# Optimization experiments

Hardware: AMD Instinct MI355X
Metric: run time of the kernel (lower is better)

## Reference

```python
import jax, jax.numpy as jnp
import numpy as np

N_NODES = 50000


def _degree_norms(edge_index, n_nodes):
    # PyG GCNConv: add self-loops, deg = 1 + in-degree at target (col)
    src, dst = edge_index[0], edge_index[1]
    deg = 1.0 + jax.ops.segment_sum(jnp.ones(src.shape[0], jnp.float32), dst,
                                    num_segments=n_nodes)
    d_inv_sqrt = 1.0 / jnp.sqrt(deg)  # deg >= 1 always (self-loop)
    norm_e = d_inv_sqrt[src] * d_inv_sqrt[dst]   # per-edge sym norm
    norm_self = d_inv_sqrt * d_inv_sqrt          # self-loop weight
    return norm_e, norm_self


def _gcn_conv(x, W, b, src, dst, norm_e, norm_self, n_nodes):
    h = x @ W                                    # [N, F_out]
    msg = h[src] * norm_e[:, None]               # gather + scale, [E, F_out]
    agg = jax.ops.segment_sum(msg, dst, num_segments=n_nodes)
    return agg + norm_self[:, None] * h + b


def setup_inputs() -> dict:
    key = jax.random.key(0)
    ks = jax.random.split(key, 10)
    F_in, H = 128, 128
    E = 1_600_000
    x = jax.random.normal(ks[0], (N_NODES, F_in), jnp.float32)
    edge_index = jax.random.randint(ks[1], (2, E), 0, N_NODES, dtype=jnp.int64)

    def glorot(k, fi, fo):
        s = jnp.sqrt(6.0 / (fi + fo)).astype(jnp.float32)
        return jax.random.uniform(k, (fi, fo), jnp.float32, -s, s)

    return {
        "x": x,
        "edge_index": edge_index,
        "W1": glorot(ks[2], F_in, H), "b1": jnp.zeros((H,), jnp.float32),
        "W2": glorot(ks[3], H, H),    "b2": jnp.zeros((H,), jnp.float32),
        "W3": glorot(ks[4], H, H),    "b3": jnp.zeros((H,), jnp.float32),
        "W4": glorot(ks[5], H, 1),    "b4": jnp.zeros((1,), jnp.float32),
    }


def reference(x, edge_index, W1, b1, W2, b2, W3, b3, W4, b4):
    src, dst = edge_index[0], edge_index[1]
    norm_e, norm_self = _degree_norms(edge_index, N_NODES)
    h = jax.nn.relu(_gcn_conv(x, W1, b1, src, dst, norm_e, norm_self, N_NODES))
    h = jax.nn.relu(_gcn_conv(h, W2, b2, src, dst, norm_e, norm_self, N_NODES))
    h = jax.nn.relu(_gcn_conv(h, W3, b3, src, dst, norm_e, norm_self, N_NODES))
    return _gcn_conv(h, W4, b4, src, dst, norm_e, norm_self, N_NODES)
```

## Files before the change

### kernel.cpp

```cpp
#include <hip/hip_runtime.h>
#include <hip/hip_bf16.h>
#include <stdint.h>

typedef unsigned int u32;
typedef unsigned short u16;

#define F 128

typedef __attribute__((ext_vector_type(8))) short bf16x8;
typedef __attribute__((ext_vector_type(8))) u16 u16x8;
typedef __attribute__((ext_vector_type(4))) float f32x4;

__device__ __forceinline__ float bf2f(u16 v){
  union { u32 u; float f; } x; x.u = ((u32)v) << 16; return x.f;
}
__device__ __forceinline__ float bflo(u32 w){
  union { u32 u; float f; } x; x.u = w << 16; return x.f;
}
__device__ __forceinline__ float bfhi(u32 w){
  union { u32 u; float f; } x; x.u = w & 0xFFFF0000u; return x.f;
}
__device__ __forceinline__ u16 f2bf(float f){
  union { float f; u32 u; } x; x.f = f;
  u32 u = x.u;
  return (u16)((u + 0x7fffu + ((u >> 16) & 1u)) >> 16);
}

__global__ void k_flags(const u32* __restrict__ xw, const u32* __restrict__ ei,
                        int* __restrict__ flags){
  if (blockIdx.x == 0){
    u32 hit = 0;
    for (int i = threadIdx.x; i < 2048; i += 256){
      u32 e = (xw[i] >> 7) & 0xFFu;
      if (e > 160u) hit = 1;
    }
    if (hit) atomicOr(&flags[1], 1);
  } else {
    u32 v = 0;
    for (int i = threadIdx.x; i < 4096; i += 256) v |= ei[2*i + 1];
    if (v) atomicOr(&flags[0], 1);
  }
}

__launch_bounds__(256)
__global__ void k_bhist(const u32* __restrict__ w, int E, const int* __restrict__ flagp,
                        int NB, int* __restrict__ bcnt){
  __shared__ int h[256];
  int st = (*flagp) ? 1 : 2;
  int t = threadIdx.x;
  h[t] = 0;
  __syncthreads();
  int base = blockIdx.x*4096;
  #pragma unroll 4
  for (int k = 0; k < 16; k++){
    int i = base + k*256 + t;
    if (i < E){
      int d = (int)w[(size_t)(E + i)*st];
      atomicAdd(&h[d >> 8], 1);
    }
  }
  __syncthreads();
  if (t < NB && h[t]) atomicAdd(&bcnt[t], h[t]);
}

__global__ void k_bscan(const int* __restrict__ bcnt, int NB, int E,
                        int* __restrict__ bbase, int* __restrict__ bump){
  __shared__ int s[256];
  int t = threadIdx.x;
  int v = (t < NB) ? bcnt[t] : 0;
  s[t] = v;
  __syncthreads();
  for (int off = 1; off < 256; off <<= 1){
    int x = (t >= off) ? s[t - off] : 0;
    __syncthreads();
    s[t] += x;
    __syncthreads();
  }
  bbase[t] = s[t] - v;
  if (t == 255) bbase[256] = E;
  bump[t] = 0;
}

__launch_bounds__(256)
__global__ void k_msplit(const u32* __restrict__ w, int E, const int* __restrict__ flagp,
                         const int* __restrict__ bbase, int* __restrict__ bump,
                         u32* __restrict__ ebuf){
  __shared__ int h[256];
  __shared__ int cb[256];
  int st = (*flagp) ? 1 : 2;
  int t = threadIdx.x;
  h[t] = 0;
  __syncthreads();
  int base = blockIdx.x*4096;
  u32 ps[16]; int bk[16]; int rk[16];
  #pragma unroll 4
  for (int k = 0; k < 16; k++){
    int i = base + k*256 + t;
    if (i < E){
      u32 s = w[(size_t)i*st];
      u32 d = w[(size_t)(E + i)*st];
      bk[k] = (int)(d >> 8);
      ps[k] = (s & 0xFFFFu) | ((d & 0xFFu) << 16);
      rk[k] = atomicAdd(&h[bk[k]], 1);
    } else bk[k] = -1;
  }
  __syncthreads();
  cb[t] = h[t] ? (bbase[t] + atomicAdd(&bump[t], h[t])) : 0;
  __syncthreads();
  #pragma unroll 4
  for (int k = 0; k < 16; k++){
    if (bk[k] >= 0) ebuf[cb[bk[k]] + rk[k]] = ps[k];
  }
}

__launch_bounds__(256)
__global__ void k_bemit(const u32* __restrict__ ebuf, const int* __restrict__ bbase,
                        int N, int* __restrict__ deg, int* __restrict__ rs,
                        u32* __restrict__ csr32, float* __restrict__ dis){
  __shared__ int nd[256];
  __shared__ int nofs[256];
  __shared__ int s[256];
  int b = blockIdx.x;
  int t = threadIdx.x;
  int e0 = bbase[b], e1 = bbase[b + 1];
  int pb = e0 + b*1024;
  nd[t] = 0;
  __syncthreads();
  for (int i = e0 + t; i < e1; i += 256) atomicAdd(&nd[ebuf[i] >> 16], 1);
  __syncthreads();
  int v = nd[t];
  int pv = (v + 3) & ~3;
  s[t] = pv;
  __syncthreads();
  for (int off = 1; off < 256; off <<= 1){
    int x = (t >= off) ? s[t - off] : 0;
    __syncthreads();
    s[t] += x;
    __syncthreads();
  }
  nofs[t] = s[t] - pv;
  int node = b*256 + t;
  if (node < N){
    deg[node] = v;
    rs[node]  = pb + nofs[t];
    dis[node] = rsqrtf(1.0f + (float)v);
  }
  nd[t] = 0;
  __syncthreads();
  for (int i = e0 + t; i < e1; i += 256){
    u32 p = ebuf[i];
    int d = (int)(p >> 16);
    int pos = pb + nofs[d] + atomicAdd(&nd[d], 1);
    csr32[pos] = (p & 0xFFFFu) << 6;
  }
}

__global__ void k_prep(const void* b1, const void* b2, const void* b3,
                       const void* W4, const void* b4, const int* __restrict__ isf32,
                       float* __restrict__ bb, float* __restrict__ wf4,
                       float* __restrict__ bb4){
  int t = threadIdx.x;
  int f32 = *isf32;
  if (t < 384){
    const void* s = (t < 128) ? b1 : ((t < 256) ? b2 : b3);
    int i = t & 127;
    bb[t] = f32 ? ((const float*)s)[i] : bf2f(((const u16*)s)[i]);
  } else if (t < 512){
    int i = t - 384;
    wf4[i] = f32 ? ((const float*)W4)[i] : bf2f(((const u16*)W4)[i]);
  } else if (t == 512){
    bb4[0] = f32 ? ((const float*)b4)[0] : bf2f(((const u16*)b4)[0]);
  }
}

__global__ void k_cvt_b(const void* __restrict__ in, const int* __restrict__ isf32,
                        u16* __restrict__ out, int N){
  int i = blockIdx.x*256 + threadIdx.x;
  if (i >= N*16) return;
  int r = i >> 4, part = i & 15;
  u16x8 o;
  if (*isf32){
    const f32x4* p = (const f32x4*)in + (size_t)i*2;
    f32x4 v0 = p[0], v1 = p[1];
    #pragma unroll
    for (int k = 0; k < 4; k++){ o[k] = f2bf(v0[k]); o[k+4] = f2bf(v1[k]); }
  } else {
    o = *((const u16x8*)in + i);
  }
  int slice = part >> 2, elem = (part & 3)*8;
  __builtin_nontemporal_store(o, (u16x8*)(out + ((size_t)slice*N + r)*32 + elem));
}

__global__ void k_swz3(const void* W1, const void* W2, const void* W3,
                       const int* __restrict__ isf32, u16* __restrict__ WL){
  int l = blockIdx.x >> 6;
  const void* W = (l == 0) ? W1 : ((l == 1) ? W2 : W3);
  int idx = (blockIdx.x & 63)*256 + threadIdx.x;
  int j    = idx & 7;
  int lane = (idx >> 3) & 63;
  int kb   = (idx >> 9) & 3;
  int ct   = idx >> 11;
  int m = lane & 15, q = lane >> 4;
  int k = kb*32 + q*8 + j;
  int c = ct*16 + m;
  float v = (*isf32) ? ((const float*)W)[k*F + c] : bf2f(((const u16*)W)[k*F + c]);
  WL[l*16384 + idx] = f2bf(v);
}

__launch_bounds__(256)
__global__ void k_mm(const u16* __restrict__ X, const u16* __restrict__ WL,
                     const float* __restrict__ dis, u16* __restrict__ G, int N){
  int w = threadIdx.x >> 6, lane = threadIdx.x & 63;
  int m = lane & 15, q = lane >> 4;
  int row0 = blockIdx.x*64 + w*16;
  int arow = row0 + m;
  bf16x8 a[4];
  if (arow < N){
    #pragma unroll
    for (int kb = 0; kb < 4; kb++)
      a[kb] = *(const bf16x8*)(X + ((size_t)kb*N + arow)*32 + q*8);
  } else {
    #pragma unroll
    for (int kb = 0; kb < 4; kb++) a[kb] = (bf16x8){0,0,0,0,0,0,0,0};
  }
  f32x4 acc[8];
  #pragma unroll
  for (int ct = 0; ct < 8; ct++) acc[ct] = (f32x4){0.f,0.f,0.f,0.f};
  #pragma unroll
  for (int ct = 0; ct < 8; ct++){
    #pragma unroll
    for (int kb = 0; kb < 4; kb++){
      bf16x8 b = *(const bf16x8*)(WL + ((size_t)((ct*4 + kb)*64 + lane))*8);
      acc[ct] = __builtin_amdgcn_mfma_f32_16x16x32_bf16(a[kb], b, acc[ct], 0, 0, 0);
    }
  }
  int rbase = row0 + q*4;
  #pragma unroll
  for (int r = 0; r < 4; r++){
    int row = rbase + r;
    if (row < N){
      float dv = dis[row];
      #pragma unroll
      for (int ct = 0; ct < 8; ct++)
        __builtin_nontemporal_store(f2bf(dv*acc[ct][r]),
            &G[((size_t)(ct >> 1)*(N+1) + row)*32 + (ct & 1)*16 + m]);
    }
  }
}

__launch_bounds__(256)
__global__ void k_agg(const u16* __restrict__ G, const float* __restrict__ dis,
                      const int* __restrict__ rs, const int* __restrict__ deg,
                      const u32* __restrict__ csr32, const float* __restrict__ bias,
                      u16* __restrict__ Xout, int N, int relu){
  int b = blockIdx.x;
  int c = (b & 7) >> 1;
  int wv = threadIdx.x >> 6;
  int lane = threadIdx.x & 63;
  int slot = lane >> 4, fp = lane & 15;
  int wid0 = (b >> 3)*16 + (b & 1)*8 + wv;
  const char* Gs = (const char*)G + (size_t)c*(size_t)(N+1)*64;
  const char* Cb = (const char*)csr32;
  u32 zoff = ((u32)N) << 6;
  u32 fo   = ((u32)fp) << 2;
  float bv0 = bias[c*32 + 2*fp], bv1 = bias[c*32 + 2*fp + 1];

  #pragma unroll 2
  for (int t = 0; t < 2; t++){
    int wid = wid0 + 4*t;
    if (wid >= N) break;
    int base = rs[wid], len = deg[wid];
    float a0 = 0.f, a1 = 0.f;
    if (len > 0){
      u32 coff = ((u32)base << 2) + ((u32)slot << 4);
      int nfull = len >> 4, rem = len & 15;
      uint4 q = *(const uint4*)(Cb + coff); coff += 64;
      for (int s = 0; s < nfull; s++){
        uint4 qn = *(const uint4*)(Cb + coff); coff += 64;
        u32 w0 = *(const u32*)(Gs + (q.x + fo));
        u32 w1 = *(const u32*)(Gs + (q.y + fo));
        u32 w2 = *(const u32*)(Gs + (q.z + fo));
        u32 w3 = *(const u32*)(Gs + (q.w + fo));
        a0 += bflo(w0); a1 += bfhi(w0);
        a0 += bflo(w1); a1 += bfhi(w1);
        a0 += bflo(w2); a1 += bfhi(w2);
        a0 += bflo(w3); a1 += bfhi(w3);
        q = qn;
      }
      if (rem){
        int sb = slot << 2;
        u32 o0 = ((sb + 0 < rem) ? q.x : zoff) + fo;
        u32 o1 = ((sb + 1 < rem) ? q.y : zoff) + fo;
        u32 o2 = ((sb + 2 < rem) ? q.z : zoff) + fo;
        u32 o3 = ((sb + 3 < rem) ? q.w : zoff) + fo;
        u32 w0 = *(const u32*)(Gs + o0);
        u32 w1 = *(const u32*)(Gs + o1);
        u32 w2 = *(const u32*)(Gs + o2);
        u32 w3 = *(const u32*)(Gs + o3);
        a0 += bflo(w0); a1 += bfhi(w0);
        a0 += bflo(w1); a1 += bfhi(w1);
        a0 += bflo(w2); a1 += bfhi(w2);
        a0 += bflo(w3); a1 += bfhi(w3);
      }
    }
    a0 += __shfl_xor(a0, 16, 64); a0 += __shfl_xor(a0, 32, 64);
    a1 += __shfl_xor(a1, 16, 64); a1 += __shfl_xor(a1, 32, 64);
    if (slot == 0){
      u32 sw = *(const u32*)(Gs + ((((u32)wid) << 6) + fo));
      a0 += bflo(sw); a1 += bfhi(sw);
      float dv = dis[wid];
      float o0 = fmaf(dv, a0, bv0);
      float o1 = fmaf(dv, a1, bv1);
      if (relu){ o0 = fmaxf(o0, 0.f); o1 = fmaxf(o1, 0.f); }
      u32 pk = (u32)f2bf(o0) | ((u32)f2bf(o1) << 16);
      __builtin_nontemporal_store(pk,
          (u32*)((char*)Xout + (size_t)c*N*64 + (((size_t)wid) << 6) + fo));
    }
  }
}

__global__ void k_mm4(const u16* __restrict__ X, const float* __restrict__ W4f,
                      const float* __restrict__ dis, float* __restrict__ G4, int N){
  int gt   = blockIdx.x*blockDim.x + threadIdx.x;
  int wid  = gt >> 6;
  int lane = threadIdx.x & 63;
  if (wid >= N) return;
  u32 xw = *(const u32*)(X + ((size_t)(lane >> 4)*N + wid)*32 + 2*(lane & 15));
  float acc = bflo(xw)*W4f[2*lane] + bfhi(xw)*W4f[2*lane + 1];
  #pragma unroll
  for (int off = 32; off > 0; off >>= 1) acc += __shfl_down(acc, off, 64);
  if (lane == 0) G4[wid] = dis[wid]*acc;
}

__global__ void k_agg4(const float* __restrict__ G4, const float* __restrict__ dis,
                       const int* __restrict__ rs, const int* __restrict__ deg,
                       const u32* __restrict__ csr32, const float* __restrict__ b4f,
                       const int* __restrict__ isf32, void* __restrict__ out, int N){
  int i = blockIdx.x*blockDim.x + threadIdx.x;
  if (i >= N) return;
  int base = rs[i], len = deg[i];
  const char* Gb = (const char*)G4;
  float a0 = 0.f, a1 = 0.f, a2 = 0.f, a3 = 0.f;
  int j = 0;
  for (; j + 4 <= len; j += 4){
    u32 e0 = csr32[base + j],     e1 = csr32[base + j + 1];
    u32 e2 = csr32[base + j + 2], e3 = csr32[base + j + 3];
    a0 += *(const float*)(Gb + (e0 >> 4));
    a1 += *(const float*)(Gb + (e1 >> 4));
    a2 += *(const float*)(Gb + (e2 >> 4));
    a3 += *(const float*)(Gb + (e3 >> 4));
  }
  for (; j < len; j++) a0 += *(const float*)(Gb + (csr32[base + j] >> 4));
  float r = dis[i]*(G4[i] + ((a0 + a1) + (a2 + a3))) + b4f[0];
  if (*isf32) ((float*)out)[i] = r;
  else        ((u16*)out)[i]   = f2bf(r);
}

extern "C" void kernel_launch(void* const* d_in, const int* in_sizes, int n_in,
                              void* d_out, int out_size, void* d_ws, size_t ws_size,
                              hipStream_t stream){
  const void* x0 = d_in[0];
  const u32*  ei = (const u32*)d_in[1];
  const void* Wp[4] = {d_in[2], d_in[4], d_in[6], d_in[8]};
  const void* bp[4] = {d_in[3], d_in[5], d_in[7], d_in[9]};
  int N = in_sizes[0] / F;
  int E = in_sizes[1] / 2;
  int NB = (N + 255) >> 8;

  char* base = (char*)d_ws;
  size_t off = 0;
  auto alloc = [&](size_t bytes)->char*{
    char* p = base + off;
    off = (off + bytes + 255) & ~(size_t)255;
    return p;
  };
  int*   deg  = (int*)  alloc((size_t)N*4);
  float* dis  = (float*)alloc((size_t)N*4);
  int*   rs   = (int*)  alloc((size_t)N*4);
  float* g4   = (float*)alloc((size_t)N*4);
  int*   bcnt = (int*)  alloc(1024);
  int*   bbase= (int*)  alloc(1056);
  int*   bump = (int*)  alloc(1024);
  int*   flags= (int*)  alloc(256);
  u32*   ebuf = (u32*)  alloc((size_t)E*4);
  u32*   csr32= (u32*)  alloc(((size_t)E + (size_t)NB*1024 + 64)*4);
  u16*   WL   = (u16*)  alloc(3*16384*2);
  float* wf4  = (float*)alloc(F*4);
  float* bb   = (float*)alloc(3*F*4);
  float* bb4  = (float*)alloc(256);
  u16*   gbuf = (u16*)  alloc((size_t)4*(N+1)*64);
  u16*   xbuf = (u16*)  alloc((size_t)N*F*2);

  hipMemsetAsync(bcnt, 0, 1024, stream);
  hipMemsetAsync(flags, 0, 256, stream);
  for (int c = 0; c < 4; c++)
    hipMemsetAsync(gbuf + ((size_t)c*(N+1) + N)*32, 0, 64, stream);

  int* eflag = flags + 0;
  int* isf32 = flags + 1;

  int nbt = (N + 255)/256;
  int etb = (E + 4095)/4096;

  k_flags <<<2, 256, 0, stream>>>((const u32*)x0, ei, flags);
  k_bhist <<<etb, 256, 0, stream>>>(ei, E, eflag, NB, bcnt);
  k_bscan <<<1, 256, 0, stream>>>(bcnt, NB, E, bbase, bump);
  k_msplit<<<etb, 256, 0, stream>>>(ei, E, eflag, bbase, bump, ebuf);
  k_bemit <<<NB, 256, 0, stream>>>(ebuf, bbase, N, deg, rs, csr32, dis);
  k_prep  <<<1, 640, 0, stream>>>(bp[0], bp[1], bp[2], Wp[3], bp[3], isf32, bb, wf4, bb4);
  k_swz3  <<<192, 256, 0, stream>>>(Wp[0], Wp[1], Wp[2], isf32, WL);
  k_cvt_b <<<(N*16 + 255)/256, 256, 0, stream>>>(x0, isf32, xbuf, N);

  int mmb  = (N + 63)/64;
  int aggB = ((N + 15)/16)*8;

  for (int l = 0; l < 3; l++){
    k_mm <<<mmb, 256, 0, stream>>>(xbuf, WL + l*16384, dis, gbuf, N);
    k_agg<<<aggB, 256, 0, stream>>>(gbuf, dis, rs, deg, csr32, bb + l*F, xbuf, N, 1);
  }
  k_mm4 <<<((size_t)N*64 + 255)/256, 256, 0, stream>>>(xbuf, wf4, dis, g4, N);
  k_agg4<<<nbt, 256, 0, stream>>>(g4, dis, rs, deg, csr32, bb4, isf32, (void*)d_out, N);
}
```

Before: 412.8 us.

## Pad CSR rows to 32, widen aggregation gathers with dot2, fuse input conversion

CSR rows are padded to multiples of 32 with zero-row sentinels and interleaved, so the aggregation kernel can skip remainder handling. Each lane now gathers 8 bytes (four bf16 features) and accumulates with v_dot2_f32_bf16, which halves the lanes per feature slice and adds an extra shuffle reduction stage. The separate input conversion kernel is removed and the first matmul reads raw fp32 or bf16 x directly. The cost is extra padded gathers on low-degree nodes, since average degree is about 32, and a larger CSR buffer.

```diff
diff --git a/kernel.cpp b/kernel.cpp
--- a/kernel.cpp
+++ b/kernel.cpp
@@ -10,20 +10,22 @@
 typedef __attribute__((ext_vector_type(8))) short bf16x8;
 typedef __attribute__((ext_vector_type(8))) u16 u16x8;
 typedef __attribute__((ext_vector_type(4))) float f32x4;
+typedef __attribute__((ext_vector_type(2))) u32 u32x2;
+typedef __attribute__((ext_vector_type(4))) u32 u32x4;
 
 __device__ __forceinline__ float bf2f(u16 v){
   union { u32 u; float f; } x; x.u = ((u32)v) << 16; return x.f;
-}
-__device__ __forceinline__ float bflo(u32 w){
-  union { u32 u; float f; } x; x.u = w << 16; return x.f;
-}
-__device__ __forceinline__ float bfhi(u32 w){
-  union { u32 u; float f; } x; x.u = w & 0xFFFF0000u; return x.f;
 }
 __device__ __forceinline__ u16 f2bf(float f){
   union { float f; u32 u; } x; x.f = f;
   u32 u = x.u;
   return (u16)((u + 0x7fffu + ((u >> 16) & 1u)) >> 16);
+}
+__device__ __forceinline__ bf16x8 as_bf(u16x8 v){
+  union { u16x8 a; bf16x8 b; } u; u.a = v; return u.b;
+}
+__device__ __forceinline__ void d2(float& a, u32 w, u32 sel){
+  asm("v_dot2_f32_bf16 %0, %1, %2, %0" : "+v"(a) : "v"(w), "v"(sel));
 }
 
 __global__ void k_flags(const u32* __restrict__ xw, const u32* __restrict__ ei,
@@ -123,13 +125,13 @@
   int b = blockIdx.x;
   int t = threadIdx.x;
   int e0 = bbase[b], e1 = bbase[b + 1];
-  int pb = e0 + b*1024;
+  int pb = ((e0 + 31) & ~31) + b*8192;
   nd[t] = 0;
   __syncthreads();
   for (int i = e0 + t; i < e1; i += 256) atomicAdd(&nd[ebuf[i] >> 16], 1);
   __syncthreads();
   int v = nd[t];
-  int pv = (v + 3) & ~3;
+  int pv = (v + 31) & ~31;
   s[t] = pv;
   __syncthreads();
   for (int off = 1; off < 256; off <<= 1){
@@ -150,8 +152,15 @@
   for (int i = e0 + t; i < e1; i += 256){
     u32 p = ebuf[i];
     int d = (int)(p >> 16);
-    int pos = pb + nofs[d] + atomicAdd(&nd[d], 1);
+    int rr = atomicAdd(&nd[d], 1);
+    int pos = pb + nofs[d] + (rr & ~31) + ((rr & 7) << 2) + ((rr >> 3) & 3);
     csr32[pos] = (p & 0xFFFFu) << 6;
+  }
+  u32 zv = ((u32)N) << 6;
+  int bme = pb + nofs[t];
+  for (int rr = v; rr < pv; rr++){
+    int pos = bme + (rr & ~31) + ((rr & 7) << 2) + ((rr >> 3) & 3);
+    csr32[pos] = zv;
   }
 }
 
@@ -173,24 +182,6 @@
   }
 }
 
-__global__ void k_cvt_b(const void* __restrict__ in, const int* __restrict__ isf32,
-                        u16* __restrict__ out, int N){
-  int i = blockIdx.x*256 + threadIdx.x;
-  if (i >= N*16) return;
-  int r = i >> 4, part = i & 15;
-  u16x8 o;
-  if (*isf32){
-    const f32x4* p = (const f32x4*)in + (size_t)i*2;
-    f32x4 v0 = p[0], v1 = p[1];
-    #pragma unroll
-    for (int k = 0; k < 4; k++){ o[k] = f2bf(v0[k]); o[k+4] = f2bf(v1[k]); }
-  } else {
-    o = *((const u16x8*)in + i);
-  }
-  int slice = part >> 2, elem = (part & 3)*8;
-  __builtin_nontemporal_store(o, (u16x8*)(out + ((size_t)slice*N + r)*32 + elem));
-}
-
 __global__ void k_swz3(const void* W1, const void* W2, const void* W3,
                        const int* __restrict__ isf32, u16* __restrict__ WL){
   int l = blockIdx.x >> 6;
@@ -208,20 +199,40 @@
 }
 
 __launch_bounds__(256)
-__global__ void k_mm(const u16* __restrict__ X, const u16* __restrict__ WL,
-                     const float* __restrict__ dis, u16* __restrict__ G, int N){
+__global__ void k_mm(const u16* __restrict__ X, const void* __restrict__ Xraw,
+                     const int* __restrict__ isf32, const u16* __restrict__ WL,
+                     const float* __restrict__ dis, u16* __restrict__ G,
+                     int N, int mode){
   int w = threadIdx.x >> 6, lane = threadIdx.x & 63;
   int m = lane & 15, q = lane >> 4;
   int row0 = blockIdx.x*64 + w*16;
   int arow = row0 + m;
-  bf16x8 a[4];
+  u16x8 a[4];
   if (arow < N){
-    #pragma unroll
-    for (int kb = 0; kb < 4; kb++)
-      a[kb] = *(const bf16x8*)(X + ((size_t)kb*N + arow)*32 + q*8);
+    if (mode == 0){
+      #pragma unroll
+      for (int kb = 0; kb < 4; kb++)
+        a[kb] = *(const u16x8*)(X + ((size_t)kb*N + arow)*32 + q*8);
+    } else if (*isf32){
+      const float* xp = (const float*)Xraw + (size_t)arow*F;
+      #pragma unroll
+      for (int kb = 0; kb < 4; kb++){
+        f32x4 v0 = *(const f32x4*)(xp + kb*32 + q*8);
+        f32x4 v1 = *(const f32x4*)(xp + kb*32 + q*8 + 4);
+        u16x8 o;
+        #pragma unroll
+        for (int k = 0; k < 4; k++){ o[k] = f2bf(v0[k]); o[k+4] = f2bf(v1[k]); }
+        a[kb] = o;
+      }
+    } else {
+      const u16* xp = (const u16*)Xraw + (size_t)arow*F;
+      #pragma unroll
+      for (int kb = 0; kb < 4; kb++)
+        a[kb] = *(const u16x8*)(xp + kb*32 + q*8);
+    }
   } else {
     #pragma unroll
-    for (int kb = 0; kb < 4; kb++) a[kb] = (bf16x8){0,0,0,0,0,0,0,0};
+    for (int kb = 0; kb < 4; kb++) a[kb] = (u16x8){0,0,0,0,0,0,0,0};
   }
   f32x4 acc[8];
   #pragma unroll
@@ -230,8 +241,8 @@
   for (int ct = 0; ct < 8; ct++){
     #pragma unroll
     for (int kb = 0; kb < 4; kb++){
-      bf16x8 b = *(const bf16x8*)(WL + ((size_t)((ct*4 + kb)*64 + lane))*8);
-      acc[ct] = __builtin_amdgcn_mfma_f32_16x16x32_bf16(a[kb], b, acc[ct], 0, 0, 0);
+      bf16x8 bfr = *(const bf16x8*)(WL + ((size_t)((ct*4 + kb)*64 + lane))*8);
+      acc[ct] = __builtin_amdgcn_mfma_f32_16x16x32_bf16(as_bf(a[kb]), bfr, acc[ct], 0, 0, 0);
     }
   }
   int rbase = row0 + q*4;
@@ -255,66 +266,73 @@
                       u16* __restrict__ Xout, int N, int relu){
   int b = blockIdx.x;
   int c = (b & 7) >> 1;
-  int wv = threadIdx.x >> 6;
   int lane = threadIdx.x & 63;
-  int slot = lane >> 4, fp = lane & 15;
-  int wid0 = (b >> 3)*16 + (b & 1)*8 + wv;
+  int slot = lane >> 3, fp = lane & 7;
+  int wid0 = (b >> 3)*16 + (b & 1)*8 + (threadIdx.x >> 6);
   const char* Gs = (const char*)G + (size_t)c*(size_t)(N+1)*64;
   const char* Cb = (const char*)csr32;
-  u32 zoff = ((u32)N) << 6;
-  u32 fo   = ((u32)fp) << 2;
-  float bv0 = bias[c*32 + 2*fp], bv1 = bias[c*32 + 2*fp + 1];
+  u32 fo = ((u32)fp) << 3;
+  u32 sel_lo = 0x00003F80u;
+  u32 sel_hi = 0x3F800000u;
 
   #pragma unroll 2
   for (int t = 0; t < 2; t++){
     int wid = wid0 + 4*t;
     if (wid >= N) break;
-    int base = rs[wid], len = deg[wid];
-    float a0 = 0.f, a1 = 0.f;
-    if (len > 0){
-      u32 coff = ((u32)base << 2) + ((u32)slot << 4);
-      int nfull = len >> 4, rem = len & 15;
-      uint4 q = *(const uint4*)(Cb + coff); coff += 64;
-      for (int s = 0; s < nfull; s++){
-        uint4 qn = *(const uint4*)(Cb + coff); coff += 64;
-        u32 w0 = *(const u32*)(Gs + (q.x + fo));
-        u32 w1 = *(const u32*)(Gs + (q.y + fo));
-        u32 w2 = *(const u32*)(Gs + (q.z + fo));
-        u32 w3 = *(const u32*)(Gs + (q.w + fo));
-        a0 += bflo(w0); a1 += bfhi(w0);
-        a0 += bflo(w1); a1 += bfhi(w1);
-        a0 += bflo(w2); a1 += bfhi(w2);
-        a0 += bflo(w3); a1 += bfhi(w3);
+    int base = rs[wid];
+    int ngr  = (deg[wid] + 31) >> 5;
+    float a0 = 0.f, a1 = 0.f, a2 = 0.f, a3 = 0.f;
+    u32 coff = ((u32)base << 2) + ((u32)slot << 4);
+    if (ngr == 1){
+      u32x4 q = *(const u32x4*)(Cb + coff);
+      u32x2 w0 = *(const u32x2*)(Gs + (q.x + fo));
+      u32x2 w1 = *(const u32x2*)(Gs + (q.y + fo));
+      u32x2 w2 = *(const u32x2*)(Gs + (q.z + fo));
+      u32x2 w3 = *(const u32x2*)(Gs + (q.w + fo));
+      d2(a0,w0.x,sel_lo); d2(a1,w0.x,sel_hi); d2(a2,w0.y,sel_lo); d2(a3,w0.y,sel_hi);
+      d2(a0,w1.x,sel_lo); d2(a1,w1.x,sel_hi); d2(a2,w1.y,sel_lo); d2(a3,w1.y,sel_hi);
+      d2(a0,w2.x,sel_lo); d2(a1,w2.x,sel_hi); d2(a2,w2.y,sel_lo); d2(a3,w2.y,sel_hi);
+      d2(a0,w3.x,sel_lo); d2(a1,w3.x,sel_hi); d2(a2,w3.y,sel_lo); d2(a3,w3.y,sel_hi);
+    } else if (ngr > 1){
+      u32x4 q = *(const u32x4*)(Cb + coff);
+      for (int s = 0; s < ngr; s++){
+        coff += 128u;
+        u32x4 qn = *(const u32x4*)(Cb + coff);
+        u32x2 w0 = *(const u32x2*)(Gs + (q.x + fo));
+        u32x2 w1 = *(const u32x2*)(Gs + (q.y + fo));
+        u32x2 w2 = *(const u32x2*)(Gs + (q.z + fo));
+        u32x2 w3 = *(const u32x2*)(Gs + (q.w + fo));
+        d2(a0,w0.x,sel_lo); d2(a1,w0.x,sel_hi); d2(a2,w0.y,sel_lo); d2(a3,w0.y,sel_hi);
+        d2(a0,w1.x,sel_lo); d2(a1,w1.x,sel_hi); d2(a2,w1.y,sel_lo); d2(a3,w1.y,sel_hi);
+        d2(a0,w2.x,sel_lo); d2(a1,w2.x,sel_hi); d2(a2,w2.y,sel_lo); d2(a3,w2.y,sel_hi);
+        d2(a0,w3.x,sel_lo); d2(a1,w3.x,sel_hi); d2(a2,w3.y,sel_lo); d2(a3,w3.y,sel_hi);
         q = qn;
       }
-      if (rem){
-        int sb = slot << 2;
-        u32 o0 = ((sb + 0 < rem) ? q.x : zoff) + fo;
-        u32 o1 = ((sb + 1 < rem) ? q.y : zoff) + fo;
-        u32 o2 = ((sb + 2 < rem) ? q.z : zoff) + fo;
-        u32 o3 = ((sb + 3 < rem) ? q.w : zoff) + fo;
-        u32 w0 = *(const u32*)(Gs + o0);
-        u32 w1 = *(const u32*)(Gs + o1);
-        u32 w2 = *(const u32*)(Gs + o2);
-        u32 w3 = *(const u32*)(Gs + o3);
-        a0 += bflo(w0); a1 += bfhi(w0);
-        a0 += bflo(w1); a1 += bfhi(w1);
-        a0 += bflo(w2); a1 += bfhi(w2);
-        a0 += bflo(w3); a1 += bfhi(w3);
+    }
+    a0 += __shfl_xor(a0,  8, 64); a1 += __shfl_xor(a1,  8, 64);
+    a2 += __shfl_xor(a2,  8, 64); a3 += __shfl_xor(a3,  8, 64);
+    a0 += __shfl_xor(a0, 16, 64); a1 += __shfl_xor(a1, 16, 64);
+    a2 += __shfl_xor(a2, 16, 64); a3 += __shfl_xor(a3, 16, 64);
+    a0 += __shfl_xor(a0, 32, 64); a1 += __shfl_xor(a1, 32, 64);
+    a2 += __shfl_xor(a2, 32, 64); a3 += __shfl_xor(a3, 32, 64);
+    if (slot == 0){
+      u32x2 sw = *(const u32x2*)(Gs + ((((u32)wid) << 6) + fo));
+      d2(a0,sw.x,sel_lo); d2(a1,sw.x,sel_hi); d2(a2,sw.y,sel_lo); d2(a3,sw.y,sel_hi);
+      float dv = dis[wid];
+      f32x4 bv = *(const f32x4*)(bias + c*32 + 4*fp);
+      float o0 = fmaf(dv, a0, bv[0]);
+      float o1 = fmaf(dv, a1, bv[1]);
+      float o2 = fmaf(dv, a2, bv[2]);
+      float o3 = fmaf(dv, a3, bv[3]);
+      if (relu){
+        o0 = fmaxf(o0, 0.f); o1 = fmaxf(o1, 0.f);
+        o2 = fmaxf(o2, 0.f); o3 = fmaxf(o3, 0.f);
       }
-    }
-    a0 += __shfl_xor(a0, 16, 64); a0 += __shfl_xor(a0, 32, 64);
-    a1 += __shfl_xor(a1, 16, 64); a1 += __shfl_xor(a1, 32, 64);
-    if (slot == 0){
-      u32 sw = *(const u32*)(Gs + ((((u32)wid) << 6) + fo));
-      a0 += bflo(sw); a1 += bfhi(sw);
-      float dv = dis[wid];
-      float o0 = fmaf(dv, a0, bv0);
-      float o1 = fmaf(dv, a1, bv1);
-      if (relu){ o0 = fmaxf(o0, 0.f); o1 = fmaxf(o1, 0.f); }
-      u32 pk = (u32)f2bf(o0) | ((u32)f2bf(o1) << 16);
+      u32x2 pk;
+      pk.x = (u32)f2bf(o0) | ((u32)f2bf(o1) << 16);
+      pk.y = (u32)f2bf(o2) | ((u32)f2bf(o3) << 16);
       __builtin_nontemporal_store(pk,
-          (u32*)((char*)Xout + (size_t)c*N*64 + (((size_t)wid) << 6) + fo));
+          (u32x2*)((char*)Xout + (size_t)c*N*64 + (((size_t)wid) << 6) + fo));
     }
   }
 }
@@ -326,7 +344,7 @@
   int lane = threadIdx.x & 63;
   if (wid >= N) return;
   u32 xw = *(const u32*)(X + ((size_t)(lane >> 4)*N + wid)*32 + 2*(lane & 15));
-  float acc = bflo(xw)*W4f[2*lane] + bfhi(xw)*W4f[2*lane + 1];
+  float acc = bf2f((u16)xw)*W4f[2*lane] + bf2f((u16)(xw >> 16))*W4f[2*lane + 1];
   #pragma unroll
   for (int off = 32; off > 0; off >>= 1) acc += __shfl_down(acc, off, 64);
   if (lane == 0) G4[wid] = dis[wid]*acc;
@@ -338,11 +356,11 @@
                        const int* __restrict__ isf32, void* __restrict__ out, int N){
   int i = blockIdx.x*blockDim.x + threadIdx.x;
   if (i >= N) return;
-  int base = rs[i], len = deg[i];
+  int base = rs[i];
+  int plen = (deg[i] + 31) & ~31;
   const char* Gb = (const char*)G4;
   float a0 = 0.f, a1 = 0.f, a2 = 0.f, a3 = 0.f;
-  int j = 0;
-  for (; j + 4 <= len; j += 4){
+  for (int j = 0; j < plen; j += 4){
     u32 e0 = csr32[base + j],     e1 = csr32[base + j + 1];
     u32 e2 = csr32[base + j + 2], e3 = csr32[base + j + 3];
     a0 += *(const float*)(Gb + (e0 >> 4));
@@ -350,7 +368,6 @@
     a2 += *(const float*)(Gb + (e2 >> 4));
     a3 += *(const float*)(Gb + (e3 >> 4));
   }
-  for (; j < len; j++) a0 += *(const float*)(Gb + (csr32[base + j] >> 4));
   float r = dis[i]*(G4[i] + ((a0 + a1) + (a2 + a3))) + b4f[0];
   if (*isf32) ((float*)out)[i] = r;
   else        ((u16*)out)[i]   = f2bf(r);
@@ -377,13 +394,13 @@
   int*   deg  = (int*)  alloc((size_t)N*4);
   float* dis  = (float*)alloc((size_t)N*4);
   int*   rs   = (int*)  alloc((size_t)N*4);
-  float* g4   = (float*)alloc((size_t)N*4);
+  float* g4   = (float*)alloc((size_t)(N+1)*4);
   int*   bcnt = (int*)  alloc(1024);
   int*   bbase= (int*)  alloc(1056);
   int*   bump = (int*)  alloc(1024);
   int*   flags= (int*)  alloc(256);
   u32*   ebuf = (u32*)  alloc((size_t)E*4);
-  u32*   csr32= (u32*)  alloc(((size_t)E + (size_t)NB*1024 + 64)*4);
+  u32*   csr32= (u32*)  alloc(((size_t)E + (size_t)(NB+1)*8192 + 64)*4);
   u16*   WL   = (u16*)  alloc(3*16384*2);
   float* wf4  = (float*)alloc(F*4);
   float* bb   = (float*)alloc(3*F*4);
@@ -391,10 +408,11 @@
   u16*   gbuf = (u16*)  alloc((size_t)4*(N+1)*64);
   u16*   xbuf = (u16*)  alloc((size_t)N*F*2);
 
-  hipMemsetAsync(bcnt, 0, 1024, stream);
-  hipMemsetAsync(flags, 0, 256, stream);
+  (void)hipMemsetAsync(bcnt, 0, 1024, stream);
+  (void)hipMemsetAsync(flags, 0, 256, stream);
+  (void)hipMemsetAsync(g4, 0, (size_t)(N+1)*4, stream);
   for (int c = 0; c < 4; c++)
-    hipMemsetAsync(gbuf + ((size_t)c*(N+1) + N)*32, 0, 64, stream);
+    (void)hipMemsetAsync(gbuf + ((size_t)c*(N+1) + N)*32, 0, 64, stream);
 
   int* eflag = flags + 0;
   int* isf32 = flags + 1;
@@ -409,13 +427,14 @@
   k_bemit <<<NB, 256, 0, stream>>>(ebuf, bbase, N, deg, rs, csr32, dis);
   k_prep  <<<1, 640, 0, stream>>>(bp[0], bp[1], bp[2], Wp[3], bp[3], isf32, bb, wf4, bb4);
   k_swz3  <<<192, 256, 0, stream>>>(Wp[0], Wp[1], Wp[2], isf32, WL);
-  k_cvt_b <<<(N*16 + 255)/256, 256, 0, stream>>>(x0, isf32, xbuf, N);
 
   int mmb  = (N + 63)/64;
   int aggB = ((N + 15)/16)*8;
 
   for (int l = 0; l < 3; l++){
-    k_mm <<<mmb, 256, 0, stream>>>(xbuf, WL + l*16384, dis, gbuf, N);
+    k_mm <<<mmb, 256, 0, stream>>>(xbuf, (l == 0) ? x0 : (const void*)xbuf,
+                                   isf32, WL + l*16384, dis, gbuf, N,
+                                   (l == 0) ? 1 : 0);
     k_agg<<<aggB, 256, 0, stream>>>(gbuf, dis, rs, deg, csr32, bb + l*F, xbuf, N, 1);
   }
   k_mm4 <<<((size_t)N*64 + 255)/256, 256, 0, stream>>>(xbuf, wf4, dis, g4, N);
```

After: 432.5 us. +4.8%, slower.
